# Kernel tuning notes

Measured on AMD Instinct MI355X. Metric: run time of the kernel, lower is better.

The kernel has to match this reference:

```python
import jax, jax.numpy as jnp
import numpy as np

D_MODEL = 1024
N_HEADS = 16
HEAD_DIM = D_MODEL // N_HEADS


def setup_inputs() -> dict:
    key = jax.random.key(0)
    ks = jax.random.split(key, 6)
    B, S = 2, 2048
    scale = 1.0 / np.sqrt(D_MODEL)
    x = jax.random.normal(ks[0], (B, S, D_MODEL), dtype=jnp.float32)
    Wq = jax.random.normal(ks[1], (D_MODEL, D_MODEL), dtype=jnp.float32) * scale
    Wk = jax.random.normal(ks[2], (D_MODEL, D_MODEL), dtype=jnp.float32) * scale
    Wv = jax.random.normal(ks[3], (D_MODEL, D_MODEL), dtype=jnp.float32) * scale
    Wo = jax.random.normal(ks[4], (D_MODEL, D_MODEL), dtype=jnp.float32) * scale
    bo = jax.random.normal(ks[5], (D_MODEL,), dtype=jnp.float32) * 0.02
    return {"x": x, "Wq": Wq, "Wk": Wk, "Wv": Wv, "Wo": Wo, "bo": bo}


def reference(x, Wq, Wk, Wv, Wo, bo):
    B, S, _ = x.shape
    H, hd = N_HEADS, HEAD_DIM
    # qkv projections (no bias, qkv_bias=False)
    q = (x @ Wq).reshape(B, S, H, hd).transpose(0, 2, 1, 3)  # [B,H,S,hd]
    k = (x @ Wk).reshape(B, S, H, hd).transpose(0, 2, 1, 3)
    v = (x @ Wv).reshape(B, S, H, hd).transpose(0, 2, 1, 3)
    scores = jnp.einsum('bhqd,bhkd->bhqk', q, k)  # [B,H,S,S]
    causal = jnp.tril(jnp.ones((S, S), dtype=bool))  # True = keep
    scores = jnp.where(causal, scores, -jnp.inf)
    weights = jax.nn.softmax(scores / np.sqrt(hd), axis=-1)
    # dropout p=0.0 -> identity
    ctx = jnp.einsum('bhqk,bhkd->bhqd', weights, v)  # [B,H,S,hd]
    ctx = ctx.transpose(0, 2, 1, 3).reshape(B, S, H * hd)
    return ctx @ Wo + bo
```

## Files before the change

### kernel.cpp

```cpp
#include <hip/hip_runtime.h>
#include <hip/hip_bf16.h>
#include <stdint.h>

#define SEQ    2048
#define BATCH  2
#define DMODEL 1024
#define NHEADS 16
#define HDIM   64
#define MROWS  (BATCH*SEQ)

typedef __attribute__((ext_vector_type(8))) short bf16x8;
typedef __attribute__((ext_vector_type(4))) float f32x4;

__device__ inline void global_to_lds16(const void* g, void* l) {
  __builtin_amdgcn_global_load_lds(
      (const __attribute__((address_space(1))) uint32_t*)g,
      (__attribute__((address_space(3))) uint32_t*)l, 16, 0, 0);
}

__device__ inline unsigned short f2bf_bits(float f) {
  __hip_bfloat16 h = __float2bfloat16(f);
  return *(unsigned short*)&h;
}

__global__ void cvt_x(const float* __restrict__ x, __hip_bfloat16* __restrict__ xb) {
  int i = (blockIdx.x * 256 + threadIdx.x) * 4;
  float4 v = *(const float4*)(x + i);
  ushort4 o;
  o.x = f2bf_bits(v.x); o.y = f2bf_bits(v.y);
  o.z = f2bf_bits(v.z); o.w = f2bf_bits(v.w);
  *(ushort4*)(xb + i) = o;
}

__global__ void trans_w(const float* __restrict__ Wq, const float* __restrict__ Wk,
                        const float* __restrict__ Wv, const float* __restrict__ Wo,
                        __hip_bfloat16* __restrict__ Wqkv_t, __hip_bfloat16* __restrict__ Wo_t) {
  __shared__ float tile[32][33];
  int z = blockIdx.z;
  const float* W = (z == 0) ? Wq : (z == 1) ? Wk : (z == 2) ? Wv : Wo;
  __hip_bfloat16* dst = (z < 3) ? (Wqkv_t + (size_t)z * 1024 * 1024) : Wo_t;
  int k0 = blockIdx.x * 32, n0 = blockIdx.y * 32;
  int tx = threadIdx.x & 31, ty = threadIdx.x >> 5;
#pragma unroll
  for (int r = 0; r < 4; r++)
    tile[ty + r * 8][tx] = W[(size_t)(k0 + ty + r * 8) * 1024 + n0 + tx];
  __syncthreads();
#pragma unroll
  for (int r = 0; r < 4; r++)
    dst[(size_t)(n0 + ty + r * 8) * 1024 + k0 + tx] = __float2bfloat16(tile[tx][ty + r * 8]);
}

__global__ void trans_v(const __hip_bfloat16* __restrict__ QKV, __hip_bfloat16* __restrict__ Vt) {
  __shared__ __hip_bfloat16 tile[64][72];
  int bh = blockIdx.y;
  int b = bh >> 4, h = bh & 15;
  int s0 = blockIdx.x * 64;
  int t = threadIdx.x;
  int r = t >> 2, cg = (t & 3) * 16;
  const __hip_bfloat16* src = QKV + ((size_t)(b * SEQ + s0 + r)) * 3072 + 2048 + h * 64 + cg;
  *(uint4*)&tile[r][cg]     = *(const uint4*)src;
  *(uint4*)&tile[r][cg + 8] = *(const uint4*)(src + 8);
  __syncthreads();
  unsigned short tmp[16];
#pragma unroll
  for (int i = 0; i < 16; i++) tmp[i] = *(const unsigned short*)&tile[cg + i][r];
  __hip_bfloat16* dst = Vt + ((size_t)bh * 64 + r) * 2048 + s0 + cg;
  *(uint4*)dst       = *(const uint4*)&tmp[0];
  *(uint4*)(dst + 8) = *(const uint4*)&tmp[8];
}

template <int TN, bool OUT_BF16, int MINW>
__global__ __launch_bounds__(256, MINW)
void gemm_kernel(const __hip_bfloat16* __restrict__ A, const __hip_bfloat16* __restrict__ Bt,
                 void* __restrict__ C, const float* __restrict__ bias, int ldc) {
  __shared__ __hip_bfloat16 Asl[128 * 32];
  __shared__ __hip_bfloat16 Bsl[TN * 32];

  const int t = threadIdx.x;
  const int lane = t & 63;
  const int w = t >> 6;
  constexpr int MI = (TN == 128) ? 4 : 2;
  const int wrow = (TN == 128) ? (w >> 1) * 64 : w * 32;
  const int wcol = (TN == 128) ? (w & 1) * 64 : 0;
  const int m0 = blockIdx.y * 128;
  const int n0 = blockIdx.x * TN;

  f32x4 acc[MI][4];
#pragma unroll
  for (int i = 0; i < MI; i++)
#pragma unroll
    for (int j = 0; j < 4; j++) acc[i][j] = (f32x4){0.f, 0.f, 0.f, 0.f};

  const int rA0 = w * 16 + (lane >> 2);
  const int kof = (lane & 3) * 8;
  const int fm = lane & 15;
  const int fk = (lane >> 4) * 8;

  for (int k0 = 0; k0 < 1024; k0 += 32) {
#pragma unroll
    for (int i = 0; i < 2; i++) {
      int r = rA0 + i * 64;
      global_to_lds16(A + (size_t)(m0 + r) * 1024 + k0 + kof, (void*)(Asl + r * 32 + kof));
    }
#pragma unroll
    for (int i = 0; i < TN / 64; i++) {
      int r = rA0 + i * 64;
      global_to_lds16(Bt + (size_t)(n0 + r) * 1024 + k0 + kof, (void*)(Bsl + r * 32 + kof));
    }
    __syncthreads();
    bf16x8 af[MI], bfr[4];
#pragma unroll
    for (int mi = 0; mi < MI; mi++)
      af[mi] = *(const bf16x8*)(Asl + (wrow + mi * 16 + fm) * 32 + fk);
#pragma unroll
    for (int ni = 0; ni < 4; ni++)
      bfr[ni] = *(const bf16x8*)(Bsl + (wcol + ni * 16 + fm) * 32 + fk);
#pragma unroll
    for (int mi = 0; mi < MI; mi++)
#pragma unroll
      for (int ni = 0; ni < 4; ni++)
        acc[mi][ni] = __builtin_amdgcn_mfma_f32_16x16x32_bf16(af[mi], bfr[ni], acc[mi][ni], 0, 0, 0);
    __syncthreads();
  }

#pragma unroll
  for (int mi = 0; mi < MI; mi++) {
    int mb = m0 + wrow + mi * 16 + (lane >> 4) * 4;
#pragma unroll
    for (int ni = 0; ni < 4; ni++) {
      int n = n0 + wcol + ni * 16 + fm;
      float bv = OUT_BF16 ? 0.f : bias[n];
#pragma unroll
      for (int r = 0; r < 4; r++) {
        if (OUT_BF16)
          ((__hip_bfloat16*)C)[(size_t)(mb + r) * ldc + n] = __float2bfloat16(acc[mi][ni][r]);
        else
          ((float*)C)[(size_t)(mb + r) * ldc + n] = acc[mi][ni][r] + bv;
      }
    }
  }
}

__global__ __launch_bounds__(256, 3)
void attn_kernel(const __hip_bfloat16* __restrict__ QKV,
                 const __hip_bfloat16* __restrict__ Vt,
                 __hip_bfloat16* __restrict__ ctx) {
  __shared__ __hip_bfloat16 Klds[2][64 * 64];
  __shared__ __hip_bfloat16 Vlds[2][64 * 64];
  __shared__ __hip_bfloat16 Plds[2][4][16 * 64];

  const int t = threadIdx.x;
  const int lane = t & 63;
  const int w = t >> 6;
  const int jb = blockIdx.x;
  const int qtab[2] = { jb, 31 - jb };
  const int bh = blockIdx.y;
  const int b = bh >> 4, h = bh & 15;
  const int fm = lane & 15;
  const int g4 = lane >> 4;
  const int fk = g4 * 8;
  const size_t rowb = (size_t)b * SEQ;
  const float c = 0.18033688011112042f;

  const int krr = lane >> 3;
  const int kjc = (lane & 7) ^ krr;

  bf16x8 qf[2][2];
#pragma unroll
  for (int hh = 0; hh < 2; hh++) {
    const __hip_bfloat16* qp = QKV + (rowb + qtab[hh] * 64 + w * 16 + fm) * 3072 + h * 64 + fk;
    bf16x8 r0 = *(const bf16x8*)qp;
    bf16x8 r1 = *(const bf16x8*)(qp + 32);
#pragma unroll
    for (int i = 0; i < 8; i++) {
      float f0 = __uint_as_float(((unsigned)(unsigned short)r0[i]) << 16) * c;
      float f1 = __uint_as_float(((unsigned)(unsigned short)r1[i]) << 16) * c;
      r0[i] = (short)f2bf_bits(f0);
      r1[i] = (short)f2bf_bits(f1);
    }
    qf[hh][0] = r0; qf[hh][1] = r1;
  }

  bf16x8 ones;
#pragma unroll
  for (int i = 0; i < 8; i++) ones[i] = (short)0x3F80;

  f32x4 acc[2][4];
  f32x4 lacc[2];
#pragma unroll
  for (int hh = 0; hh < 2; hh++) {
    lacc[hh] = (f32x4){0.f, 0.f, 0.f, 0.f};
#pragma unroll
    for (int d = 0; d < 4; d++) acc[hh][d] = (f32x4){0.f, 0.f, 0.f, 0.f};
  }

  auto stage = [&](int kts, int bufi) {
    const int kt0 = kts * 64;
#pragma unroll
    for (int i = 0; i < 2; i++) {
      int seg = w + i * 4;
      int r = seg * 8 + krr;
      global_to_lds16(QKV + (rowb + kt0 + r) * 3072 + 1024 + h * 64 + kjc * 8,
                      (void*)(&Klds[bufi][0] + seg * 512 + lane * 8));
      global_to_lds16(Vt + ((size_t)bh * 64 + r) * 2048 + kt0 + kjc * 8,
                      (void*)(&Vlds[bufi][0] + seg * 512 + lane * 8));
    }
  };

  const int lastt = qtab[1];
  stage(0, 0);
  for (int kts = 0; kts <= lastt; ++kts) {
    __syncthreads();
    if (kts < lastt) stage(kts + 1, (kts + 1) & 1);
    const __hip_bfloat16* Kb = &Klds[kts & 1][0];
    const __hip_bfloat16* Vb = &Vlds[kts & 1][0];
    const bool act0 = (kts <= qtab[0]);

    f32x4 st1[4], st0[4];
#pragma unroll
    for (int ns = 0; ns < 4; ns++) {
      st1[ns] = (f32x4){0.f, 0.f, 0.f, 0.f};
      st0[ns] = (f32x4){0.f, 0.f, 0.f, 0.f};
    }
#pragma unroll
    for (int kk = 0; kk < 2; kk++) {
      bf16x8 kf[4];
#pragma unroll
      for (int ns = 0; ns < 4; ns++)
        kf[ns] = *(const bf16x8*)(Kb + (ns * 16 + fm) * 64 + (((kk * 4 + g4) ^ (fm & 7)) << 3));
#pragma unroll
      for (int ns = 0; ns < 4; ns++)
        st1[ns] = __builtin_amdgcn_mfma_f32_16x16x32_bf16(kf[ns], qf[1][kk], st1[ns], 0, 0, 0);
      if (act0)
#pragma unroll
        for (int ns = 0; ns < 4; ns++)
          st0[ns] = __builtin_amdgcn_mfma_f32_16x16x32_bf16(kf[ns], qf[0][kk], st0[ns], 0, 0, 0);
    }

    auto half = [&](const f32x4 (&st)[4], int hh) {
      const bool diag = (kts == qtab[hh]);
      __hip_bfloat16* Pw = &Plds[hh][w][0];
#pragma unroll
      for (int ns = 0; ns < 4; ns++) {
        unsigned short u[4];
#pragma unroll
        for (int r = 0; r < 4; r++) {
          int ktl = ns * 16 + g4 * 4 + r;
          bool msk = diag && (ktl > w * 16 + fm);
          float p = msk ? 0.f : __builtin_amdgcn_exp2f(st[ns][r]);
          u[r] = f2bf_bits(p);
        }
        int c16 = (ns * 2 + (g4 >> 1)) ^ (fm & 7);
        *(uint2*)(Pw + fm * 64 + c16 * 8 + (g4 & 1) * 4) = *(const uint2*)u;
      }
#pragma unroll
      for (int kk = 0; kk < 2; kk++) {
        bf16x8 pa = *(const bf16x8*)(Pw + fm * 64 + (((kk * 4 + g4) ^ (fm & 7)) << 3));
        lacc[hh] = __builtin_amdgcn_mfma_f32_16x16x32_bf16(pa, ones, lacc[hh], 0, 0, 0);
#pragma unroll
        for (int dd = 0; dd < 4; dd++) {
          bf16x8 vf = *(const bf16x8*)(Vb + (dd * 16 + fm) * 64 + (((kk * 4 + g4) ^ (fm & 7)) << 3));
          acc[hh][dd] = __builtin_amdgcn_mfma_f32_16x16x32_bf16(pa, vf, acc[hh][dd], 0, 0, 0);
        }
      }
    };
    half(st1, 1);
    if (act0) half(st0, 0);
  }

#pragma unroll
  for (int hh = 0; hh < 2; hh++) {
    float rl[4];
#pragma unroll
    for (int r = 0; r < 4; r++) rl[r] = __builtin_amdgcn_rcpf(lacc[hh][r]);
#pragma unroll
    for (int dd = 0; dd < 4; dd++)
#pragma unroll
      for (int r = 0; r < 4; r++) {
        int q = qtab[hh] * 64 + w * 16 + g4 * 4 + r;
        ctx[(rowb + q) * 1024 + h * 64 + dd * 16 + fm] =
            __float2bfloat16(acc[hh][dd][r] * rl[r]);
      }
  }
}

extern "C" void kernel_launch(void* const* d_in, const int* in_sizes, int n_in,
                              void* d_out, int out_size, void* d_ws, size_t ws_size,
                              hipStream_t stream) {
  const float* x  = (const float*)d_in[0];
  const float* Wq = (const float*)d_in[1];
  const float* Wk = (const float*)d_in[2];
  const float* Wv = (const float*)d_in[3];
  const float* Wo = (const float*)d_in[4];
  const float* bo = (const float*)d_in[5];
  float* out = (float*)d_out;

  char* ws = (char*)d_ws;
  __hip_bfloat16* xb     = (__hip_bfloat16*)(ws);
  __hip_bfloat16* Wqkv_t = (__hip_bfloat16*)(ws + (8ull  << 20));
  __hip_bfloat16* Wo_t   = (__hip_bfloat16*)(ws + (14ull << 20));
  __hip_bfloat16* QKV    = (__hip_bfloat16*)(ws + (16ull << 20));
  __hip_bfloat16* ctxb   = (__hip_bfloat16*)(ws + (40ull << 20));
  __hip_bfloat16* Vt     = xb;

  cvt_x<<<dim3(MROWS * DMODEL / (256 * 4)), dim3(256), 0, stream>>>(x, xb);
  trans_w<<<dim3(32, 32, 4), dim3(256), 0, stream>>>(Wq, Wk, Wv, Wo, Wqkv_t, Wo_t);
  gemm_kernel<128, true, 3><<<dim3(24, 32), dim3(256), 0, stream>>>(xb, Wqkv_t, (void*)QKV, nullptr, 3072);
  trans_v<<<dim3(32, 32), dim3(256), 0, stream>>>(QKV, Vt);
  attn_kernel<<<dim3(16, 32), dim3(256), 0, stream>>>(QKV, Vt, ctxb);
  gemm_kernel<64, false, 2><<<dim3(16, 32), dim3(256), 0, stream>>>(ctxb, Wo_t, (void*)out, bo, 1024);
}
```

Baseline: 189.0 us.

## Keep P in registers for PV MFMA and deepen GEMM K-tile

```diff
diff --git a/kernel.cpp b/kernel.cpp
--- a/kernel.cpp
+++ b/kernel.cpp
@@ -10,6 +10,7 @@
 #define MROWS  (BATCH*SEQ)
 
 typedef __attribute__((ext_vector_type(8))) short bf16x8;
+typedef __attribute__((ext_vector_type(4))) short bf16x4;
 typedef __attribute__((ext_vector_type(4))) float f32x4;
 
 __device__ inline void global_to_lds16(const void* g, void* l) {
@@ -73,8 +74,8 @@
 __global__ __launch_bounds__(256, MINW)
 void gemm_kernel(const __hip_bfloat16* __restrict__ A, const __hip_bfloat16* __restrict__ Bt,
                  void* __restrict__ C, const float* __restrict__ bias, int ldc) {
-  __shared__ __hip_bfloat16 Asl[128 * 32];
-  __shared__ __hip_bfloat16 Bsl[TN * 32];
+  __shared__ __hip_bfloat16 Asl[128 * 64];
+  __shared__ __hip_bfloat16 Bsl[TN * 64];
 
   const int t = threadIdx.x;
   const int lane = t & 63;
@@ -91,41 +92,52 @@
 #pragma unroll
     for (int j = 0; j < 4; j++) acc[i][j] = (f32x4){0.f, 0.f, 0.f, 0.f};
 
-  const int rA0 = w * 16 + (lane >> 2);
-  const int kof = (lane & 3) * 8;
+  const int srow = lane >> 3;
+  const int sjc = (lane & 7) ^ srow;
   const int fm = lane & 15;
-  const int fk = (lane >> 4) * 8;
-
-  for (int k0 = 0; k0 < 1024; k0 += 32) {
-#pragma unroll
-    for (int i = 0; i < 2; i++) {
-      int r = rA0 + i * 64;
-      global_to_lds16(A + (size_t)(m0 + r) * 1024 + k0 + kof, (void*)(Asl + r * 32 + kof));
-    }
-#pragma unroll
-    for (int i = 0; i < TN / 64; i++) {
-      int r = rA0 + i * 64;
-      global_to_lds16(Bt + (size_t)(n0 + r) * 1024 + k0 + kof, (void*)(Bsl + r * 32 + kof));
+  const int g4 = lane >> 4;
+
+  for (int k0 = 0; k0 < 1024; k0 += 64) {
+#pragma unroll
+    for (int i = 0; i < 4; i++) {
+      int seg = i * 4 + w;
+      int r = seg * 8 + srow;
+      global_to_lds16(A + (size_t)(m0 + r) * 1024 + k0 + sjc * 8,
+                      (void*)(Asl + seg * 512 + lane * 8));
+    }
+#pragma unroll
+    for (int i = 0; i < TN / 32; i++) {
+      int seg = i * 4 + w;
+      int r = seg * 8 + srow;
+      global_to_lds16(Bt + (size_t)(n0 + r) * 1024 + k0 + sjc * 8,
+                      (void*)(Bsl + seg * 512 + lane * 8));
     }
     __syncthreads();
-    bf16x8 af[MI], bfr[4];
-#pragma unroll
-    for (int mi = 0; mi < MI; mi++)
-      af[mi] = *(const bf16x8*)(Asl + (wrow + mi * 16 + fm) * 32 + fk);
-#pragma unroll
-    for (int ni = 0; ni < 4; ni++)
-      bfr[ni] = *(const bf16x8*)(Bsl + (wcol + ni * 16 + fm) * 32 + fk);
-#pragma unroll
-    for (int mi = 0; mi < MI; mi++)
-#pragma unroll
-      for (int ni = 0; ni < 4; ni++)
-        acc[mi][ni] = __builtin_amdgcn_mfma_f32_16x16x32_bf16(af[mi], bfr[ni], acc[mi][ni], 0, 0, 0);
+#pragma unroll
+    for (int kb = 0; kb < 2; kb++) {
+      bf16x8 af[MI], bfr[4];
+#pragma unroll
+      for (int mi = 0; mi < MI; mi++) {
+        int row = wrow + mi * 16 + fm;
+        af[mi] = *(const bf16x8*)(Asl + row * 64 + (((kb * 4 + g4) ^ (row & 7)) << 3));
+      }
+#pragma unroll
+      for (int ni = 0; ni < 4; ni++) {
+        int row = wcol + ni * 16 + fm;
+        bfr[ni] = *(const bf16x8*)(Bsl + row * 64 + (((kb * 4 + g4) ^ (row & 7)) << 3));
+      }
+#pragma unroll
+      for (int mi = 0; mi < MI; mi++)
+#pragma unroll
+        for (int ni = 0; ni < 4; ni++)
+          acc[mi][ni] = __builtin_amdgcn_mfma_f32_16x16x32_bf16(af[mi], bfr[ni], acc[mi][ni], 0, 0, 0);
+    }
     __syncthreads();
   }
 
 #pragma unroll
   for (int mi = 0; mi < MI; mi++) {
-    int mb = m0 + wrow + mi * 16 + (lane >> 4) * 4;
+    int mb = m0 + wrow + mi * 16 + g4 * 4;
 #pragma unroll
     for (int ni = 0; ni < 4; ni++) {
       int n = n0 + wcol + ni * 16 + fm;
@@ -147,7 +159,6 @@
                  __hip_bfloat16* __restrict__ ctx) {
   __shared__ __hip_bfloat16 Klds[2][64 * 64];
   __shared__ __hip_bfloat16 Vlds[2][64 * 64];
-  __shared__ __hip_bfloat16 Plds[2][4][16 * 64];
 
   const int t = threadIdx.x;
   const int lane = t & 63;
@@ -181,9 +192,9 @@
     qf[hh][0] = r0; qf[hh][1] = r1;
   }
 
-  bf16x8 ones;
-#pragma unroll
-  for (int i = 0; i < 8; i++) ones[i] = (short)0x3F80;
+  bf16x4 ones4;
+#pragma unroll
+  for (int i = 0; i < 4; i++) ones4[i] = (short)0x3F80;
 
   f32x4 acc[2][4];
   f32x4 lacc[2];
@@ -237,9 +248,16 @@
           st0[ns] = __builtin_amdgcn_mfma_f32_16x16x32_bf16(kf[ns], qf[0][kk], st0[ns], 0, 0, 0);
     }
 
+    bf16x4 vf[4][4];
+#pragma unroll
+    for (int dd = 0; dd < 4; dd++)
+#pragma unroll
+      for (int ns = 0; ns < 4; ns++)
+        vf[dd][ns] = *(const bf16x4*)(Vb + (dd * 16 + fm) * 64 +
+                                      (((2 * ns + (g4 >> 1)) ^ (fm & 7)) << 3) + (g4 & 1) * 4);
+
     auto half = [&](const f32x4 (&st)[4], int hh) {
       const bool diag = (kts == qtab[hh]);
-      __hip_bfloat16* Pw = &Plds[hh][w][0];
 #pragma unroll
       for (int ns = 0; ns < 4; ns++) {
         unsigned short u[4];
@@ -250,18 +268,11 @@
           float p = msk ? 0.f : __builtin_amdgcn_exp2f(st[ns][r]);
           u[r] = f2bf_bits(p);
         }
-        int c16 = (ns * 2 + (g4 >> 1)) ^ (fm & 7);
-        *(uint2*)(Pw + fm * 64 + c16 * 8 + (g4 & 1) * 4) = *(const uint2*)u;
-      }
-#pragma unroll
-      for (int kk = 0; kk < 2; kk++) {
-        bf16x8 pa = *(const bf16x8*)(Pw + fm * 64 + (((kk * 4 + g4) ^ (fm & 7)) << 3));
-        lacc[hh] = __builtin_amdgcn_mfma_f32_16x16x32_bf16(pa, ones, lacc[hh], 0, 0, 0);
-#pragma unroll
-        for (int dd = 0; dd < 4; dd++) {
-          bf16x8 vf = *(const bf16x8*)(Vb + (dd * 16 + fm) * 64 + (((kk * 4 + g4) ^ (fm & 7)) << 3));
-          acc[hh][dd] = __builtin_amdgcn_mfma_f32_16x16x32_bf16(pa, vf, acc[hh][dd], 0, 0, 0);
-        }
+        bf16x4 pf = *(const bf16x4*)u;
+        lacc[hh] = __builtin_amdgcn_mfma_f32_16x16x16bf16_1k(pf, ones4, lacc[hh], 0, 0, 0);
+#pragma unroll
+        for (int dd = 0; dd < 4; dd++)
+          acc[hh][dd] = __builtin_amdgcn_mfma_f32_16x16x16bf16_1k(pf, vf[dd][ns], acc[hh][dd], 0, 0, 0);
       }
     };
     half(st1, 1);
```

Result: faster. 180.5 us (-4.5%).
